# Kernel optimization log

Hardware: AMD Instinct MI355X
Metric: run time of the kernel (lower is better)

Reference implementation:

```python
import jax, jax.numpy as jnp
import numpy as np

D_STATE = 16
D_CONV = 4


def rmsnorm(x, w, eps=1e-6):
    # normalize over last (channel) axis
    return x * jax.lax.rsqrt(jnp.mean(x * x, axis=-1, keepdims=True) + eps) * w


def silu(x):
    return x * jax.nn.sigmoid(x)


def mamba(x, in_proj_w, conv1d_w, conv1d_b, x_proj_w, dt_proj_w, dt_proj_b, A_log, D_param, out_proj_w):
    # x: [B, L, C], d_inner == C (expand=1)
    B, L, C = x.shape
    dt_rank = dt_proj_w.shape[1]
    xz = jnp.einsum('blc,ec->ble', x, in_proj_w)  # [B, L, 2C]
    u, z = jnp.split(xz, 2, axis=-1)
    # causal depthwise conv1d over time (pad left d_conv-1)
    uc = jax.lax.conv_general_dilated(
        u.transpose(0, 2, 1), conv1d_w[:, None, :], (1,), [(D_CONV - 1, 0)],
        dimension_numbers=('NCH', 'OIH', 'NCH'), feature_group_count=C)
    u = silu((uc + conv1d_b[None, :, None]).transpose(0, 2, 1))  # [B, L, C]
    x_dbl = jnp.einsum('blc,ec->ble', u, x_proj_w)  # [B, L, dt_rank + 2*N]
    dt, Bm, Cm = jnp.split(x_dbl, [dt_rank, dt_rank + D_STATE], axis=-1)
    delta = jax.nn.softplus(jnp.einsum('blr,dr->bld', dt, dt_proj_w) + dt_proj_b)  # [B, L, C]
    A = -jnp.exp(A_log)  # [C, N]
    deltaA = jnp.exp(delta[..., None] * A)              # [B, L, C, N]
    deltaBu = (delta * u)[..., None] * Bm[:, :, None, :]  # [B, L, C, N]

    def step(h, inp):
        dA, dBu, c = inp
        h = dA * h + dBu
        return h, jnp.einsum('bdn,bn->bd', h, c)

    h0 = jnp.zeros((B, C, D_STATE), x.dtype)
    _, ys = jax.lax.scan(step, h0, (deltaA.transpose(1, 0, 2, 3),
                                    deltaBu.transpose(1, 0, 2, 3),
                                    Cm.transpose(1, 0, 2)))
    y = ys.transpose(1, 0, 2) + u * D_param  # [B, L, C]
    y = y * silu(z)
    return jnp.einsum('bld,od->blo', y, out_proj_w)


def reference(x, norm_w, in_proj_w, conv1d_w, conv1d_b, x_proj_w, dt_proj_w, dt_proj_b,
              A_log, D_param, out_proj_w, scale_mod, dw_w, dw_b, res_scale):
    B, C, H, W = x.shape
    x_cl = x.transpose(0, 2, 3, 1)              # [B, H, W, C]
    xn_cl = rmsnorm(x_cl, norm_w)
    x_norm = xn_cl.transpose(0, 3, 1, 2)        # [B, C, H, W]
    # bidirectional Mamba over flattened spatial sequence
    x_flat = xn_cl.reshape(B, H * W, C)
    mparams = (in_proj_w, conv1d_w, conv1d_b, x_proj_w, dt_proj_w, dt_proj_b, A_log, D_param, out_proj_w)
    fwd = mamba(x_flat, *mparams)
    bwd = jnp.flip(mamba(jnp.flip(x_flat, axis=1), *mparams), axis=1)
    g = (fwd + bwd) * scale_mod
    global_feat = g.reshape(B, H, W, C).transpose(0, 3, 1, 2)
    # local spatial gating: sigmoid(depthwise 3x3 conv) * x_norm
    conv = jax.lax.conv_general_dilated(
        x_norm, dw_w[:, None, :, :], (1, 1), [(1, 1), (1, 1)],
        dimension_numbers=('NCHW', 'OIHW', 'NCHW'), feature_group_count=C)
    local_feat = jax.nn.sigmoid(conv + dw_b[None, :, None, None]) * x_norm
    return x + res_scale * (global_feat + local_feat)


def setup_inputs() -> dict:
    key = jax.random.key(0)
    ks = jax.random.split(key, 10)
    B, C, H, W = 8, 384, 32, 32
    dt_rank = 24  # ceil(384 / 16)
    s = 0.02
    f32 = jnp.float32
    return {
        'x': jax.random.normal(ks[0], (B, C, H, W), f32),
        'norm_w': jnp.ones((C,), f32),
        'in_proj_w': jax.random.normal(ks[1], (2 * C, C), f32) * s,
        'conv1d_w': jax.random.normal(ks[2], (C, D_CONV), f32) * 0.2,
        'conv1d_b': jnp.zeros((C,), f32),
        'x_proj_w': jax.random.normal(ks[3], (dt_rank + 2 * D_STATE, C), f32) * s,
        'dt_proj_w': jax.random.normal(ks[4], (C, dt_rank), f32) * 0.1,
        'dt_proj_b': jax.random.uniform(ks[5], (C,), f32, -4.0, -2.0),
        'A_log': jnp.log(jnp.tile(jnp.arange(1, D_STATE + 1, dtype=f32), (C, 1))),
        'D_param': jnp.ones((C,), f32),
        'out_proj_w': jax.random.normal(ks[6], (C, C), f32) * s,
        'scale_mod': jnp.full((1,), 0.25, f32),
        'dw_w': jax.random.normal(ks[7], (C, 3, 3), f32) * 0.1,
        'dw_b': jnp.zeros((C,), f32),
        'res_scale': jnp.full((1,), 0.5, f32),
    }
```

## Files before the change

kernel.cpp:

```cpp
#include <hip/hip_runtime.h>
#include <hip/hip_bf16.h>


typedef __attribute__((ext_vector_type(8))) short bf16x8;
typedef __attribute__((ext_vector_type(8))) unsigned short u16x8;
typedef __attribute__((ext_vector_type(4))) float f32x4;

#define L2E 1.44269504088896340736f

static __device__ __forceinline__ unsigned short f2bf(float f) {
  unsigned int u = __builtin_bit_cast(unsigned int, f);
  u += 0x7fff + ((u >> 16) & 1);
  return (unsigned short)(u >> 16);
}
static __device__ __forceinline__ float bf2f(unsigned short u) {
  unsigned int v = (unsigned int)u << 16;
  return __builtin_bit_cast(float, v);
}

__global__ __launch_bounds__(256) void prep_k(
    const float* __restrict__ in_w, const float* __restrict__ x_w,
    const float* __restrict__ dt_w, const float* __restrict__ out_w,
    const float* __restrict__ A_log, const float* __restrict__ nw,
    unsigned short* __restrict__ W_in, unsigned short* __restrict__ W_x,
    unsigned short* __restrict__ W_dt, unsigned short* __restrict__ W_out,
    float* __restrict__ A2) {
  int idx = blockIdx.x * 256 + threadIdx.x;
  switch (blockIdx.y) {
    case 0: if (idx < 768 * 384) W_in[idx] = f2bf(in_w[idx] * nw[idx % 384]); break;
    case 1: if (idx < 64 * 384) { int n = idx / 384, k = idx - n * 384;
              W_x[idx] = f2bf(n < 56 ? x_w[n * 384 + k] : 0.f); } break;
    case 2: if (idx < 384 * 32) { int n = idx >> 5, k = idx & 31;
              W_dt[idx] = f2bf(k < 24 ? dt_w[n * 24 + k] : 0.f); } break;
    case 3: if (idx < 384 * 384) W_out[idx] = f2bf(out_w[idx]); break;
    case 4: if (idx < 384 * 16) A2[idx] = -expf(A_log[idx]) * L2E; break;
  }
}

__global__ __launch_bounds__(256) void transpose_k(
    const float* __restrict__ x, unsigned short* __restrict__ xb,
    float* __restrict__ nf) {
  const int b = blockIdx.y;
  const int l0 = blockIdx.x * 32;
  const int tid = threadIdx.x;
  const int cr = tid >> 5, lw = tid & 31;
  const int cj = tid & 63, lr = tid >> 6;
  __shared__ float t64[64][33];
  __shared__ float part[8][33];
  float acc = 0.f;
  for (int cc = 0; cc < 6; ++cc) {
    #pragma unroll
    for (int k = 0; k < 8; ++k) {
      int cp = k * 8 + cr;
      int c = cc * 64 + cp;
      float v = x[(((size_t)(b * 384 + c)) << 10) + l0 + lw];
      t64[cp][lw] = v;
      acc = fmaf(v, v, acc);
    }
    __syncthreads();
    #pragma unroll
    for (int k2 = 0; k2 < 8; ++k2) {
      int ll = lr + 4 * k2;
      xb[((size_t)((b << 10) + l0 + ll)) * 384 + cc * 64 + cj] = f2bf(t64[cj][ll]);
    }
    __syncthreads();
  }
  part[cr][lw] = acc;
  __syncthreads();
  if (tid < 32) {
    float s = part[0][tid] + part[1][tid] + part[2][tid] + part[3][tid] +
              part[4][tid] + part[5][tid] + part[6][tid] + part[7][tid];
    nf[(b << 10) + l0 + tid] = rsqrtf(s * (1.f / 384.f) + 1e-6f);
  }
}

template <int EPI, int SUMIN>
__global__ __launch_bounds__(256) void gemm_k(
    const unsigned short* __restrict__ A0u, const unsigned short* __restrict__ A1u,
    const unsigned short* __restrict__ Bw, int K, int N,
    float* __restrict__ of0, float* __restrict__ of1,
    unsigned short* __restrict__ ob0, unsigned short* __restrict__ ob1,
    const float* __restrict__ aux) {
  const unsigned short* A = blockIdx.z ? A1u : A0u;
  float* outf = blockIdx.z ? of1 : of0;
  unsigned short* outb = blockIdx.z ? ob1 : ob0;
  __shared__ unsigned short As[64][40];
  __shared__ unsigned short Bs[64][40];
  const int n0 = blockIdx.x * 64, m0 = blockIdx.y * 64;
  const int tid = threadIdx.x;
  const int lane = tid & 63, wave = tid >> 6;
  const int wm = wave >> 1, wn = wave & 1;
  const int lrow = tid >> 2, lseg = (tid & 3) * 8;
  const int fr = lane & 15, ks = (lane >> 4) * 8;
  f32x4 acc[2][2] = {};
  for (int k0 = 0; k0 < K; k0 += 32) {
    __syncthreads();
    if (SUMIN) {
      u16x8 va = *(const u16x8*)&A0u[(size_t)(m0 + lrow) * K + k0 + lseg];
      u16x8 vb = *(const u16x8*)&A1u[(size_t)(m0 + lrow) * K + k0 + lseg];
      u16x8 s;
      #pragma unroll
      for (int j = 0; j < 8; ++j) s[j] = f2bf(bf2f(va[j]) + bf2f(vb[j]));
      *(u16x8*)&As[lrow][lseg] = s;
    } else {
      *(bf16x8*)&As[lrow][lseg] = *(const bf16x8*)&A[(size_t)(m0 + lrow) * K + k0 + lseg];
    }
    *(bf16x8*)&Bs[lrow][lseg] = *(const bf16x8*)&Bw[(size_t)(n0 + lrow) * K + k0 + lseg];
    __syncthreads();
    bf16x8 a0 = *(const bf16x8*)&As[wm * 32 + fr][ks];
    bf16x8 a1 = *(const bf16x8*)&As[wm * 32 + 16 + fr][ks];
    bf16x8 b0 = *(const bf16x8*)&Bs[wn * 32 + fr][ks];
    bf16x8 b1 = *(const bf16x8*)&Bs[wn * 32 + 16 + fr][ks];
    acc[0][0] = __builtin_amdgcn_mfma_f32_16x16x32_bf16(a0, b0, acc[0][0], 0, 0, 0);
    acc[0][1] = __builtin_amdgcn_mfma_f32_16x16x32_bf16(a0, b1, acc[0][1], 0, 0, 0);
    acc[1][0] = __builtin_amdgcn_mfma_f32_16x16x32_bf16(a1, b0, acc[1][0], 0, 0, 0);
    acc[1][1] = __builtin_amdgcn_mfma_f32_16x16x32_bf16(a1, b1, acc[1][1], 0, 0, 0);
  }
  #pragma unroll
  for (int mi = 0; mi < 2; ++mi)
    #pragma unroll
    for (int ni = 0; ni < 2; ++ni)
      #pragma unroll
      for (int j = 0; j < 4; ++j) {
        int m = m0 + wm * 32 + mi * 16 + (lane >> 4) * 4 + j;
        int n = n0 + wn * 32 + ni * 16 + (lane & 15);
        float v = acc[mi][ni][j];
        if (EPI == 0) {
          ob0[(size_t)m * N + n] = f2bf(v * aux[m]);
        } else if (EPI == 1) {
          if (n < 24) outb[m * 32 + n] = f2bf(v);
          else if (n < 32) outb[m * 32 + n] = 0;
          if (n >= 24 && n < 56) outf[m * 32 + (n - 24)] = v;
        } else if (EPI == 2) {
          float t = v + aux[n];
          float sp = (t > 20.f) ? t : log1pf(expf(t));
          outb[(size_t)m * N + n] = f2bf(sp);
        } else {
          of0[(size_t)m * N + n] = v * aux[0];
        }
      }
}

__global__ __launch_bounds__(384) void conv_silu_k(
    const unsigned short* __restrict__ xz, const float* __restrict__ cw,
    const float* __restrict__ cb,
    unsigned short* __restrict__ ub0, unsigned short* __restrict__ ub1) {
  const int st = blockIdx.x, b = blockIdx.y, dir = blockIdx.z;
  const int c = threadIdx.x;
  const int s0 = st * 8;
  const float w0 = cw[c * 4 + 0], w1 = cw[c * 4 + 1];
  const float w2 = cw[c * 4 + 2], w3 = cw[c * 4 + 3];
  const float bb = cb[c];
  unsigned short* ub = dir ? ub1 : ub0;
  float xv[11];
  #pragma unroll
  for (int k = 0; k < 11; ++k) {
    int j = s0 - 3 + k;
    float v = 0.f;
    if (j >= 0) {
      int t = dir ? (1023 - j) : j;
      v = bf2f(xz[(size_t)((b << 10) + t) * 768 + c]);
    }
    xv[k] = v;
  }
  #pragma unroll
  for (int s = 0; s < 8; ++s) {
    float a = bb + xv[s] * w0 + xv[s + 1] * w1 + xv[s + 2] * w2 + xv[s + 3] * w3;
    float uv = a * __builtin_amdgcn_rcpf(1.f + __builtin_amdgcn_exp2f(-a * L2E));
    ub[(size_t)((b << 10) + s0 + s) * 384 + c] = f2bf(uv);
  }
}

__global__ __launch_bounds__(512) void scan1_k(
    const unsigned short* __restrict__ de0, const unsigned short* __restrict__ de1,
    const unsigned short* __restrict__ ub0, const unsigned short* __restrict__ ub1,
    const float* __restrict__ bc0, const float* __restrict__ bc1,
    const float* __restrict__ A2,
    float* __restrict__ Pseg, float* __restrict__ Hseg) {
  const int ct = blockIdx.x, b = blockIdx.y;
  const int dir = blockIdx.z >> 4, seg = blockIdx.z & 15;
  const unsigned short* del = dir ? de1 : de0;
  const unsigned short* uu  = dir ? ub1 : ub0;
  const float* bc  = dir ? bc1 : bc0;
  const int tid = threadIdx.x;
  const int lane = tid & 63, wave = tid >> 6;
  const int n = lane & 15, cg = lane >> 4;
  const int cl = wave * 4 + cg;
  const int c = ct * 32 + cl;
  const float a2 = A2[c * 16 + n];
  const size_t base = ((size_t)b << 10) + seg * 64;
  __shared__ __attribute__((aligned(16))) float sd[2][32][20];
  __shared__ __attribute__((aligned(16))) float sdu[2][32][20];
  __shared__ __attribute__((aligned(16))) float sB[2][32][20];
  const int li = tid >> 5, lj = tid & 31;
  unsigned short rd, ru; float rb;
  auto issue = [&](int s0) {
    size_t rowi = base + s0 + li;
    rd = del[rowi * 384 + ct * 32 + lj];
    ru = uu [rowi * 384 + ct * 32 + lj];
    rb = bc [rowi * 32 + lj];
  };
  auto commit = [&](int buf) {
    float dd = bf2f(rd), uv = bf2f(ru);
    sd[buf][lj][li] = dd; sdu[buf][lj][li] = dd * uv; sB[buf][lj][li] = rb;
  };
  issue(0); commit(0);
  float h = 0.f, P = 1.f;
  for (int ch = 0; ch < 4; ++ch) {
    const int cur = ch & 1;
    if (ch + 1 < 4) issue((ch + 1) * 16);
    __syncthreads();
    f32x4 dv[4], duv[4], bmv[4];
    #pragma unroll
    for (int r = 0; r < 4; ++r) {
      dv[r]  = *(const f32x4*)&sd[cur][cl][r * 4];
      duv[r] = *(const f32x4*)&sdu[cur][cl][r * 4];
      bmv[r] = *(const f32x4*)&sB[cur][n][r * 4];
    }
    #pragma unroll
    for (int i = 0; i < 16; ++i) {
      float dA = __builtin_amdgcn_exp2f(dv[i >> 2][i & 3] * a2);
      h = fmaf(dA, h, duv[i >> 2][i & 3] * bmv[i >> 2][i & 3]);
      P *= dA;
    }
    if (ch + 1 < 4) { __syncthreads(); commit(cur ^ 1); }
  }
  size_t o = (size_t)((dir * 8 + b) * 16 + seg) * 6144 + c * 16 + n;
  Pseg[o] = P; Hseg[o] = h;
}

__global__ __launch_bounds__(256) void scomb_k(
    const float* __restrict__ Pseg, const float* __restrict__ Hseg,
    float* __restrict__ Hin) {
  const int db = blockIdx.y;
  const int r = blockIdx.x * 256 + threadIdx.x;
  float h = 0.f;
  #pragma unroll
  for (int s = 0; s < 16; ++s) {
    size_t o = (size_t)(db * 16 + s) * 6144 + r;
    Hin[o] = h;
    h = Pseg[o] * h + Hseg[o];
  }
}

__global__ __launch_bounds__(512) void scan2_k(
    const unsigned short* __restrict__ de0, const unsigned short* __restrict__ de1,
    const unsigned short* __restrict__ ub0, const unsigned short* __restrict__ ub1,
    const float* __restrict__ bc0, const float* __restrict__ bc1,
    const unsigned short* __restrict__ xz, const float* __restrict__ A2,
    const float* __restrict__ Dp, const float* __restrict__ Hin,
    unsigned short* __restrict__ Sb0, unsigned short* __restrict__ Sb1) {
  const int ct = blockIdx.x, b = blockIdx.y;
  const int dir = blockIdx.z >> 4, seg = blockIdx.z & 15;
  const unsigned short* del = dir ? de1 : de0;
  const unsigned short* uu  = dir ? ub1 : ub0;
  const float* bc  = dir ? bc1 : bc0;
  unsigned short* S = dir ? Sb1 : Sb0;
  const int tid = threadIdx.x;
  const int lane = tid & 63, wave = tid >> 6;
  const int n = lane & 15, cg = lane >> 4;
  const int cl = wave * 4 + cg;
  const int c = ct * 32 + cl;
  const float a2 = A2[c * 16 + n];
  const float dpc = Dp[c];
  const size_t base = (size_t)b << 10;
  const int segoff = seg * 64;
  __shared__ __attribute__((aligned(16))) float sd[2][32][20];
  __shared__ __attribute__((aligned(16))) float sdu[2][32][20];
  __shared__ __attribute__((aligned(16))) float su[2][32][20];
  __shared__ __attribute__((aligned(16))) float sz[2][32][20];
  __shared__ __attribute__((aligned(16))) float sbc[2][32][20];
  const int li = tid >> 5, lj = tid & 31;
  unsigned short rd, ru, rz; float rb;
  auto issue = [&](int s0) {
    size_t rowi = base + segoff + s0 + li;
    rd = del[rowi * 384 + ct * 32 + lj];
    ru = uu [rowi * 384 + ct * 32 + lj];
    int t = dir ? (1023 - (segoff + s0 + li)) : (segoff + s0 + li);
    rz = xz[(base + t) * 768 + 384 + ct * 32 + lj];
    rb = bc[rowi * 32 + lj];
  };
  auto commit = [&](int buf) {
    float dd = bf2f(rd), uv = bf2f(ru);
    sd[buf][lj][li] = dd; sdu[buf][lj][li] = dd * uv;
    su[buf][lj][li] = uv; sz[buf][lj][li] = bf2f(rz);
    sbc[buf][lj][li] = rb;
  };
  issue(0); commit(0);
  float h = Hin[(size_t)((dir * 8 + b) * 16 + seg) * 6144 + c * 16 + n];
  for (int ch = 0; ch < 4; ++ch) {
    const int cur = ch & 1;
    if (ch + 1 < 4) issue((ch + 1) * 16);
    __syncthreads();
    f32x4 dv[4], duv[4], bmv[4], cmv[4];
    #pragma unroll
    for (int r = 0; r < 4; ++r) {
      dv[r]  = *(const f32x4*)&sd[cur][cl][r * 4];
      duv[r] = *(const f32x4*)&sdu[cur][cl][r * 4];
      bmv[r] = *(const f32x4*)&sbc[cur][n][r * 4];
      cmv[r] = *(const f32x4*)&sbc[cur][16 + n][r * 4];
    }
    float p[16];
    #pragma unroll
    for (int i = 0; i < 16; ++i) {
      float dA = __builtin_amdgcn_exp2f(dv[i >> 2][i & 3] * a2);
      h = fmaf(dA, h, duv[i >> 2][i & 3] * bmv[i >> 2][i & 3]);
      p[i] = h * cmv[i >> 2][i & 3];
    }
    float q8[8];
    #pragma unroll
    for (int j = 0; j < 8; ++j) {
      float send = (n & 8) ? p[j] : p[j + 8];
      float recv = __shfl_xor(send, 8);
      float keep = (n & 8) ? p[j + 8] : p[j];
      q8[j] = keep + recv;
    }
    float q4[4];
    #pragma unroll
    for (int j = 0; j < 4; ++j) {
      float send = (n & 4) ? q8[j] : q8[j + 4];
      float recv = __shfl_xor(send, 4);
      float keep = (n & 4) ? q8[j + 4] : q8[j];
      q4[j] = keep + recv;
    }
    float q2[2];
    #pragma unroll
    for (int j = 0; j < 2; ++j) {
      float send = (n & 2) ? q4[j] : q4[j + 2];
      float recv = __shfl_xor(send, 2);
      float keep = (n & 2) ? q4[j + 2] : q4[j];
      q2[j] = keep + recv;
    }
    float send = (n & 1) ? q2[0] : q2[1];
    float recv = __shfl_xor(send, 1);
    float keep = (n & 1) ? q2[1] : q2[0];
    float ysum = keep + recv;
    float uvn = su[cur][cl][n];
    float zz  = sz[cur][cl][n];
    float sig = __builtin_amdgcn_rcpf(1.f + __builtin_amdgcn_exp2f(-zz * L2E));
    float y = (ysum + uvn * dpc) * (zz * sig);
    int s = segoff + ch * 16 + n;
    int t = dir ? (1023 - s) : s;
    S[(base + t) * 384 + c] = f2bf(y);
    if (ch + 1 < 4) { __syncthreads(); commit(cur ^ 1); }
  }
}

__global__ __launch_bounds__(256) void final_k(
    const float* __restrict__ G, const unsigned short* __restrict__ xb,
    const float* __restrict__ nf, const float* __restrict__ nw,
    const float* __restrict__ x, const float* __restrict__ dww,
    const float* __restrict__ dwb, const float* __restrict__ rs,
    float* __restrict__ out) {
  __shared__ float tile[64][33];
  __shared__ float wq[9][64];
  __shared__ float bbs[64], nws[64];
  const int l0 = blockIdx.x * 32, c0 = blockIdx.y * 64, b = blockIdx.z;
  const int tid = threadIdx.x;
  for (int i = tid; i < 576; i += 256) {
    int c = i / 9, q = i - c * 9;
    wq[q][c] = dww[(size_t)(c0 + c) * 9 + q] * nw[c0 + c];
  }
  if (tid < 64) { bbs[tid] = dwb[c0 + tid]; nws[tid] = nw[c0 + tid]; }
  __syncthreads();
  {
    const int oct = tid & 7, li = tid >> 3;
    const int l = l0 + li;
    const int hh = l >> 5, ww = l & 31;
    float acc[8];
    {
      f32x4 ba = *(const f32x4*)&bbs[oct * 8];
      f32x4 bb2 = *(const f32x4*)&bbs[oct * 8 + 4];
      #pragma unroll
      for (int j = 0; j < 4; ++j) { acc[j] = ba[j]; acc[j + 4] = bb2[j]; }
    }
    #pragma unroll
    for (int di = -1; di <= 1; ++di) {
      int h2 = hh + di;
      if (h2 < 0 || h2 > 31) continue;
      #pragma unroll
      for (int dj = -1; dj <= 1; ++dj) {
        int w2 = ww + dj;
        if (w2 < 0 || w2 > 31) continue;
        int lp = h2 * 32 + w2;
        float nfl = nf[(b << 10) + lp];
        u16x8 v = *(const u16x8*)&xb[(size_t)((b << 10) + lp) * 384 + c0 + oct * 8];
        int q = (di + 1) * 3 + (dj + 1);
        f32x4 wa = *(const f32x4*)&wq[q][oct * 8];
        f32x4 wb = *(const f32x4*)&wq[q][oct * 8 + 4];
        #pragma unroll
        for (int j = 0; j < 4; ++j) {
          acc[j]     = fmaf(bf2f(v[j]) * nfl, wa[j], acc[j]);
          acc[j + 4] = fmaf(bf2f(v[j + 4]) * nfl, wb[j], acc[j + 4]);
        }
      }
    }
    size_t ri = (size_t)((b << 10) + l) * 384 + c0 + oct * 8;
    float nfl0 = nf[(b << 10) + l];
    u16x8 xc = *(const u16x8*)&xb[ri];
    f32x4 g0 = *(const f32x4*)&G[ri];
    f32x4 g1 = *(const f32x4*)&G[ri + 4];
    #pragma unroll
    for (int j = 0; j < 8; ++j) {
      float xv = bf2f(xc[j]) * nfl0 * nws[oct * 8 + j];
      float sig = __builtin_amdgcn_rcpf(1.f + __builtin_amdgcn_exp2f(-acc[j] * L2E));
      float gg = (j < 4) ? g0[j] : g1[j - 4];
      tile[oct * 8 + j][li] = gg + xv * sig;
    }
  }
  __syncthreads();
  {
    const int lw = tid & 31, cr = tid >> 5;
    const float rsv = rs[0];
    for (int p = 0; p < 8; ++p) {
      int c = c0 + p * 8 + cr;
      size_t o = ((size_t)(b * 384 + c) << 10) + l0 + lw;
      out[o] = x[o] + rsv * tile[p * 8 + cr][lw];
    }
  }
}

extern "C" void kernel_launch(void* const* d_in, const int* in_sizes, int n_in,
                              void* d_out, int out_size, void* d_ws, size_t ws_size,
                              hipStream_t stream) {
  const float* x         = (const float*)d_in[0];
  const float* norm_w    = (const float*)d_in[1];
  const float* in_proj_w = (const float*)d_in[2];
  const float* conv1d_w  = (const float*)d_in[3];
  const float* conv1d_b  = (const float*)d_in[4];
  const float* x_proj_w  = (const float*)d_in[5];
  const float* dt_proj_w = (const float*)d_in[6];
  const float* dt_proj_b = (const float*)d_in[7];
  const float* A_log     = (const float*)d_in[8];
  const float* D_param   = (const float*)d_in[9];
  const float* out_proj_w= (const float*)d_in[10];
  const float* scale_mod = (const float*)d_in[11];
  const float* dw_w      = (const float*)d_in[12];
  const float* dw_b      = (const float*)d_in[13];
  const float* res_scale = (const float*)d_in[14];
  float* out = (float*)d_out;

  char* base = (char*)d_ws;
  size_t off = 0;
  auto alloc = [&](size_t bytes) {
    off = (off + 255) & ~(size_t)255;
    void* p = base + off;
    off += bytes;
    return p;
  };
  const size_t B_BLC = (size_t)8192 * 384 * 2;

  unsigned short* xb   = (unsigned short*)alloc(B_BLC);
  float*          nf   = (float*)alloc((size_t)8192 * 4);
  unsigned short* xz   = (unsigned short*)alloc((size_t)8192 * 768 * 2);
  unsigned short* u_b0 = (unsigned short*)alloc(B_BLC);
  unsigned short* u_b1 = (unsigned short*)alloc(B_BLC);
  unsigned short* dtp0 = (unsigned short*)alloc((size_t)8192 * 32 * 2);
  unsigned short* dtp1 = (unsigned short*)alloc((size_t)8192 * 32 * 2);
  float*          bc0  = (float*)alloc((size_t)8192 * 32 * 4);
  float*          bc1  = (float*)alloc((size_t)8192 * 32 * 4);
  unsigned short* de0  = (unsigned short*)alloc(B_BLC);
  unsigned short* de1  = (unsigned short*)alloc(B_BLC);
  unsigned short* Sb0  = (unsigned short*)alloc(B_BLC);
  unsigned short* Sb1  = (unsigned short*)alloc(B_BLC);
  float*          Pseg = (float*)alloc((size_t)1572864 * 4);
  float*          Hseg = (float*)alloc((size_t)1572864 * 4);
  float*          Hin  = (float*)alloc((size_t)1572864 * 4);
  unsigned short* W_in = (unsigned short*)alloc((size_t)768 * 384 * 2);
  unsigned short* W_x  = (unsigned short*)alloc((size_t)64 * 384 * 2);
  unsigned short* W_dt = (unsigned short*)alloc((size_t)384 * 32 * 2);
  unsigned short* W_out= (unsigned short*)alloc((size_t)384 * 384 * 2);
  float*          A2   = (float*)alloc((size_t)384 * 16 * 4);
  float*          G    = (float*)alloc((size_t)8192 * 384 * 4);

  prep_k<<<dim3(1152, 5), 256, 0, stream>>>(in_proj_w, x_proj_w, dt_proj_w,
                                            out_proj_w, A_log, norm_w,
                                            W_in, W_x, W_dt, W_out, A2);
  transpose_k<<<dim3(32, 8), 256, 0, stream>>>(x, xb, nf);
  gemm_k<0, 0><<<dim3(12, 128), 256, 0, stream>>>(xb, xb, W_in, 384, 768,
                                                  nullptr, nullptr, xz, xz, nf);
  conv_silu_k<<<dim3(128, 8, 2), 384, 0, stream>>>(xz, conv1d_w, conv1d_b,
                                                   u_b0, u_b1);
  gemm_k<1, 0><<<dim3(1, 128, 2), 256, 0, stream>>>(u_b0, u_b1, W_x, 384, 64,
                                                    bc0, bc1, dtp0, dtp1, nullptr);
  gemm_k<2, 0><<<dim3(6, 128, 2), 256, 0, stream>>>(dtp0, dtp1, W_dt, 32, 384,
                                                    nullptr, nullptr, de0, de1,
                                                    dt_proj_b);
  scan1_k<<<dim3(12, 8, 32), 512, 0, stream>>>(de0, de1, u_b0, u_b1, bc0, bc1,
                                               A2, Pseg, Hseg);
  scomb_k<<<dim3(24, 16), 256, 0, stream>>>(Pseg, Hseg, Hin);
  scan2_k<<<dim3(12, 8, 32), 512, 0, stream>>>(de0, de1, u_b0, u_b1, bc0, bc1,
                                               xz, A2, D_param, Hin, Sb0, Sb1);
  gemm_k<3, 1><<<dim3(6, 128), 256, 0, stream>>>(Sb0, Sb1, W_out, 384, 384,
                                                 G, G, nullptr, nullptr,
                                                 scale_mod);
  final_k<<<dim3(32, 6, 8), 256, 0, stream>>>(G, xb, nf, norm_w, x, dw_w, dw_b,
                                              res_scale, out);
}
```

Baseline: 257.8 us.

## Use 128x128 MFMA GEMM with direct LDS loads, fold scan combine into scan2

Adds a 128x128-tile bf16 MFMA GEMM that moves A/B tiles straight into LDS with global_load_lds and computes a 4x4 fragment grid per wave. It is used for the in_proj and out_proj GEMMs to raise data reuse and arithmetic intensity. The scan kernels now load a whole 64-step segment into LDS once instead of double-buffering 16-step chunks, and compute delta*u on the fly. The separate segment-combine kernel is removed: scan2 rebuilds its starting state from packed (P,h) pairs of the earlier segments, which cuts a launch at the cost of redundant per-thread work and fewer CTAs for the GEMMs.

Result: faster. 247.3 us (-4.0%).

```diff
diff --git a/kernel.cpp b/kernel.cpp
--- a/kernel.cpp
+++ b/kernel.cpp
@@ -17,6 +17,11 @@
   unsigned int v = (unsigned int)u << 16;
   return __builtin_bit_cast(float, v);
 }
+
+#define GLOAD_LDS16(g, l)                                             \
+  __builtin_amdgcn_global_load_lds(                                   \
+      (const __attribute__((address_space(1))) unsigned int*)(g),     \
+      (__attribute__((address_space(3))) unsigned int*)(l), 16, 0, 0)
 
 __global__ __launch_bounds__(256) void prep_k(
     const float* __restrict__ in_w, const float* __restrict__ x_w,
@@ -75,6 +80,81 @@
 }
 
 template <int EPI, int SUMIN>
+__global__ __launch_bounds__(256) void gemm128_k(
+    const unsigned short* __restrict__ A0u, const unsigned short* __restrict__ A1u,
+    const unsigned short* __restrict__ Bw, int K, int N,
+    float* __restrict__ outf, unsigned short* __restrict__ outb,
+    const float* __restrict__ aux) {
+  __shared__ __attribute__((aligned(16))) unsigned short As[128 * 32];
+  __shared__ __attribute__((aligned(16))) unsigned short Bs[128 * 32];
+  const int n0 = blockIdx.x * 128, m0 = blockIdx.y * 128;
+  const int tid = threadIdx.x;
+  const int lane = tid & 63, wave = tid >> 6;
+  const int wm = wave >> 1, wn = wave & 1;
+  const int fr = lane & 15, ks = (lane >> 4) * 8;
+  const int row = tid >> 2, colseg = (tid & 3) * 8;
+  const unsigned short* pA0 = A0u + (size_t)(m0 + row) * K + colseg;
+  const unsigned short* pA1 = A0u + (size_t)(m0 + 64 + row) * K + colseg;
+  const unsigned short* pB0 = Bw + (size_t)(n0 + row) * K + colseg;
+  const unsigned short* pB1 = Bw + (size_t)(n0 + 64 + row) * K + colseg;
+  unsigned short* lA0 = As + wave * 512;
+  unsigned short* lA1 = As + 2048 + wave * 512;
+  unsigned short* lB0 = Bs + wave * 512;
+  unsigned short* lB1 = Bs + 2048 + wave * 512;
+  f32x4 acc[4][4] = {};
+  for (int k0 = 0; k0 < K; k0 += 32) {
+    __syncthreads();
+    if (SUMIN) {
+      #pragma unroll
+      for (int p = 0; p < 2; ++p) {
+        int r = p * 64 + row;
+        u16x8 va = *(const u16x8*)&A0u[(size_t)(m0 + r) * K + k0 + colseg];
+        u16x8 vb = *(const u16x8*)&A1u[(size_t)(m0 + r) * K + k0 + colseg];
+        u16x8 s;
+        #pragma unroll
+        for (int j = 0; j < 8; ++j) s[j] = f2bf(bf2f(va[j]) + bf2f(vb[j]));
+        *(u16x8*)&As[r * 32 + colseg] = s;
+      }
+    } else {
+      GLOAD_LDS16(pA0, lA0);
+      GLOAD_LDS16(pA1, lA1);
+      pA0 += 32; pA1 += 32;
+    }
+    GLOAD_LDS16(pB0, lB0);
+    GLOAD_LDS16(pB1, lB1);
+    pB0 += 32; pB1 += 32;
+    __syncthreads();
+    bf16x8 af[4], bf[4];
+    #pragma unroll
+    for (int mi = 0; mi < 4; ++mi)
+      af[mi] = *(const bf16x8*)&As[(wm * 64 + mi * 16 + fr) * 32 + ks];
+    #pragma unroll
+    for (int ni = 0; ni < 4; ++ni)
+      bf[ni] = *(const bf16x8*)&Bs[(wn * 64 + ni * 16 + fr) * 32 + ks];
+    #pragma unroll
+    for (int mi = 0; mi < 4; ++mi)
+      #pragma unroll
+      for (int ni = 0; ni < 4; ++ni)
+        acc[mi][ni] = __builtin_amdgcn_mfma_f32_16x16x32_bf16(af[mi], bf[ni], acc[mi][ni], 0, 0, 0);
+  }
+  #pragma unroll
+  for (int mi = 0; mi < 4; ++mi)
+    #pragma unroll
+    for (int ni = 0; ni < 4; ++ni)
+      #pragma unroll
+      for (int j = 0; j < 4; ++j) {
+        int m = m0 + wm * 64 + mi * 16 + (lane >> 4) * 4 + j;
+        int n = n0 + wn * 64 + ni * 16 + fr;
+        float v = acc[mi][ni][j];
+        if (EPI == 0) {
+          outb[(size_t)m * N + n] = f2bf(v * aux[m]);
+        } else {
+          outf[(size_t)m * N + n] = v * aux[0];
+        }
+      }
+}
+
+template <int EPI>
 __global__ __launch_bounds__(256) void gemm_k(
     const unsigned short* __restrict__ A0u, const unsigned short* __restrict__ A1u,
     const unsigned short* __restrict__ Bw, int K, int N,
@@ -95,16 +175,7 @@
   f32x4 acc[2][2] = {};
   for (int k0 = 0; k0 < K; k0 += 32) {
     __syncthreads();
-    if (SUMIN) {
-      u16x8 va = *(const u16x8*)&A0u[(size_t)(m0 + lrow) * K + k0 + lseg];
-      u16x8 vb = *(const u16x8*)&A1u[(size_t)(m0 + lrow) * K + k0 + lseg];
-      u16x8 s;
-      #pragma unroll
-      for (int j = 0; j < 8; ++j) s[j] = f2bf(bf2f(va[j]) + bf2f(vb[j]));
-      *(u16x8*)&As[lrow][lseg] = s;
-    } else {
-      *(bf16x8*)&As[lrow][lseg] = *(const bf16x8*)&A[(size_t)(m0 + lrow) * K + k0 + lseg];
-    }
+    *(bf16x8*)&As[lrow][lseg] = *(const bf16x8*)&A[(size_t)(m0 + lrow) * K + k0 + lseg];
     *(bf16x8*)&Bs[lrow][lseg] = *(const bf16x8*)&Bw[(size_t)(n0 + lrow) * K + k0 + lseg];
     __syncthreads();
     bf16x8 a0 = *(const bf16x8*)&As[wm * 32 + fr][ks];
@@ -125,18 +196,14 @@
         int m = m0 + wm * 32 + mi * 16 + (lane >> 4) * 4 + j;
         int n = n0 + wn * 32 + ni * 16 + (lane & 15);
         float v = acc[mi][ni][j];
-        if (EPI == 0) {
-          ob0[(size_t)m * N + n] = f2bf(v * aux[m]);
-        } else if (EPI == 1) {
+        if (EPI == 1) {
           if (n < 24) outb[m * 32 + n] = f2bf(v);
           else if (n < 32) outb[m * 32 + n] = 0;
           if (n >= 24 && n < 56) outf[m * 32 + (n - 24)] = v;
-        } else if (EPI == 2) {
+        } else {
           float t = v + aux[n];
           float sp = (t > 20.f) ? t : log1pf(expf(t));
           outb[(size_t)m * N + n] = f2bf(sp);
-        } else {
-          of0[(size_t)m * N + n] = v * aux[0];
         }
       }
 }
@@ -175,8 +242,7 @@
     const unsigned short* __restrict__ de0, const unsigned short* __restrict__ de1,
     const unsigned short* __restrict__ ub0, const unsigned short* __restrict__ ub1,
     const float* __restrict__ bc0, const float* __restrict__ bc1,
-    const float* __restrict__ A2,
-    float* __restrict__ Pseg, float* __restrict__ Hseg) {
+    const float* __restrict__ A2, float* __restrict__ PH) {
   const int ct = blockIdx.x, b = blockIdx.y;
   const int dir = blockIdx.z >> 4, seg = blockIdx.z & 15;
   const unsigned short* del = dir ? de1 : de0;
@@ -189,58 +255,49 @@
   const int c = ct * 32 + cl;
   const float a2 = A2[c * 16 + n];
   const size_t base = ((size_t)b << 10) + seg * 64;
-  __shared__ __attribute__((aligned(16))) float sd[2][32][20];
-  __shared__ __attribute__((aligned(16))) float sdu[2][32][20];
-  __shared__ __attribute__((aligned(16))) float sB[2][32][20];
+  __shared__ __attribute__((aligned(16))) float sd[32][68];
+  __shared__ __attribute__((aligned(16))) float su[32][68];
+  __shared__ __attribute__((aligned(16))) float sB[16][68];
   const int li = tid >> 5, lj = tid & 31;
-  unsigned short rd, ru; float rb;
-  auto issue = [&](int s0) {
-    size_t rowi = base + s0 + li;
-    rd = del[rowi * 384 + ct * 32 + lj];
-    ru = uu [rowi * 384 + ct * 32 + lj];
-    rb = bc [rowi * 32 + lj];
-  };
-  auto commit = [&](int buf) {
-    float dd = bf2f(rd), uv = bf2f(ru);
-    sd[buf][lj][li] = dd; sdu[buf][lj][li] = dd * uv; sB[buf][lj][li] = rb;
-  };
-  issue(0); commit(0);
+  const int li3 = tid >> 4, lj3 = tid & 15;
+  unsigned short rd[4], ru[4];
+  float rb[2];
+  #pragma unroll
+  for (int k = 0; k < 4; ++k) {
+    size_t rowi = base + k * 16 + li;
+    rd[k] = del[rowi * 384 + ct * 32 + lj];
+    ru[k] = uu [rowi * 384 + ct * 32 + lj];
+  }
+  #pragma unroll
+  for (int k = 0; k < 2; ++k)
+    rb[k] = bc[(base + k * 32 + li3) * 32 + lj3];
+  #pragma unroll
+  for (int k = 0; k < 4; ++k) {
+    sd[lj][k * 16 + li] = bf2f(rd[k]);
+    su[lj][k * 16 + li] = bf2f(ru[k]);
+  }
+  #pragma unroll
+  for (int k = 0; k < 2; ++k) sB[lj3][k * 32 + li3] = rb[k];
+  __syncthreads();
   float h = 0.f, P = 1.f;
   for (int ch = 0; ch < 4; ++ch) {
-    const int cur = ch & 1;
-    if (ch + 1 < 4) issue((ch + 1) * 16);
-    __syncthreads();
-    f32x4 dv[4], duv[4], bmv[4];
+    f32x4 dv[4], uv4[4], bmv[4];
     #pragma unroll
     for (int r = 0; r < 4; ++r) {
-      dv[r]  = *(const f32x4*)&sd[cur][cl][r * 4];
-      duv[r] = *(const f32x4*)&sdu[cur][cl][r * 4];
-      bmv[r] = *(const f32x4*)&sB[cur][n][r * 4];
+      dv[r]  = *(const f32x4*)&sd[cl][ch * 16 + r * 4];
+      uv4[r] = *(const f32x4*)&su[cl][ch * 16 + r * 4];
+      bmv[r] = *(const f32x4*)&sB[n][ch * 16 + r * 4];
     }
     #pragma unroll
     for (int i = 0; i < 16; ++i) {
-      float dA = __builtin_amdgcn_exp2f(dv[i >> 2][i & 3] * a2);
-      h = fmaf(dA, h, duv[i >> 2][i & 3] * bmv[i >> 2][i & 3]);
+      float dd = dv[i >> 2][i & 3];
+      float dA = __builtin_amdgcn_exp2f(dd * a2);
+      h = fmaf(dA, h, dd * uv4[i >> 2][i & 3] * bmv[i >> 2][i & 3]);
       P *= dA;
     }
-    if (ch + 1 < 4) { __syncthreads(); commit(cur ^ 1); }
   }
   size_t o = (size_t)((dir * 8 + b) * 16 + seg) * 6144 + c * 16 + n;
-  Pseg[o] = P; Hseg[o] = h;
-}
-
-__global__ __launch_bounds__(256) void scomb_k(
-    const float* __restrict__ Pseg, const float* __restrict__ Hseg,
-    float* __restrict__ Hin) {
-  const int db = blockIdx.y;
-  const int r = blockIdx.x * 256 + threadIdx.x;
-  float h = 0.f;
-  #pragma unroll
-  for (int s = 0; s < 16; ++s) {
-    size_t o = (size_t)(db * 16 + s) * 6144 + r;
-    Hin[o] = h;
-    h = Pseg[o] * h + Hseg[o];
-  }
+  *(float2*)&PH[o * 2] = make_float2(P, h);
 }
 
 __global__ __launch_bounds__(512) void scan2_k(
@@ -248,7 +305,7 @@
     const unsigned short* __restrict__ ub0, const unsigned short* __restrict__ ub1,
     const float* __restrict__ bc0, const float* __restrict__ bc1,
     const unsigned short* __restrict__ xz, const float* __restrict__ A2,
-    const float* __restrict__ Dp, const float* __restrict__ Hin,
+    const float* __restrict__ Dp, const float* __restrict__ PH,
     unsigned short* __restrict__ Sb0, unsigned short* __restrict__ Sb1) {
   const int ct = blockIdx.x, b = blockIdx.y;
   const int dir = blockIdx.z >> 4, seg = blockIdx.z & 15;
@@ -265,46 +322,54 @@
   const float dpc = Dp[c];
   const size_t base = (size_t)b << 10;
   const int segoff = seg * 64;
-  __shared__ __attribute__((aligned(16))) float sd[2][32][20];
-  __shared__ __attribute__((aligned(16))) float sdu[2][32][20];
-  __shared__ __attribute__((aligned(16))) float su[2][32][20];
-  __shared__ __attribute__((aligned(16))) float sz[2][32][20];
-  __shared__ __attribute__((aligned(16))) float sbc[2][32][20];
+  __shared__ __attribute__((aligned(16))) float sd[32][68];
+  __shared__ __attribute__((aligned(16))) float su[32][68];
+  __shared__ __attribute__((aligned(16))) float sz[32][68];
+  __shared__ __attribute__((aligned(16))) float sbc[32][68];
   const int li = tid >> 5, lj = tid & 31;
-  unsigned short rd, ru, rz; float rb;
-  auto issue = [&](int s0) {
-    size_t rowi = base + segoff + s0 + li;
-    rd = del[rowi * 384 + ct * 32 + lj];
-    ru = uu [rowi * 384 + ct * 32 + lj];
-    int t = dir ? (1023 - (segoff + s0 + li)) : (segoff + s0 + li);
-    rz = xz[(base + t) * 768 + 384 + ct * 32 + lj];
-    rb = bc[rowi * 32 + lj];
-  };
-  auto commit = [&](int buf) {
-    float dd = bf2f(rd), uv = bf2f(ru);
-    sd[buf][lj][li] = dd; sdu[buf][lj][li] = dd * uv;
-    su[buf][lj][li] = uv; sz[buf][lj][li] = bf2f(rz);
-    sbc[buf][lj][li] = rb;
-  };
-  issue(0); commit(0);
-  float h = Hin[(size_t)((dir * 8 + b) * 16 + seg) * 6144 + c * 16 + n];
+  unsigned short rd[4], ru[4], rz[4];
+  float rb[4];
+  #pragma unroll
+  for (int k = 0; k < 4; ++k) {
+    size_t rowi = base + segoff + k * 16 + li;
+    rd[k] = del[rowi * 384 + ct * 32 + lj];
+    ru[k] = uu [rowi * 384 + ct * 32 + lj];
+    int t = dir ? (1023 - (segoff + k * 16 + li)) : (segoff + k * 16 + li);
+    rz[k] = xz[(base + t) * 768 + 384 + ct * 32 + lj];
+    rb[k] = bc[rowi * 32 + lj];
+  }
+  float h = 0.f;
+  {
+    size_t rb2 = ((size_t)((dir * 8 + b) * 16) * 6144 + c * 16 + n) * 2;
+    #pragma unroll
+    for (int s = 0; s < 15; ++s) {
+      float2 ph = *(const float2*)&PH[rb2 + (size_t)s * 12288];
+      h = (s < seg) ? fmaf(ph.x, h, ph.y) : h;
+    }
+  }
+  #pragma unroll
+  for (int k = 0; k < 4; ++k) {
+    sd[lj][k * 16 + li] = bf2f(rd[k]);
+    su[lj][k * 16 + li] = bf2f(ru[k]);
+    sz[lj][k * 16 + li] = bf2f(rz[k]);
+    sbc[lj][k * 16 + li] = rb[k];
+  }
+  __syncthreads();
   for (int ch = 0; ch < 4; ++ch) {
-    const int cur = ch & 1;
-    if (ch + 1 < 4) issue((ch + 1) * 16);
-    __syncthreads();
-    f32x4 dv[4], duv[4], bmv[4], cmv[4];
+    f32x4 dv[4], uv4[4], bmv[4], cmv[4];
     #pragma unroll
     for (int r = 0; r < 4; ++r) {
-      dv[r]  = *(const f32x4*)&sd[cur][cl][r * 4];
-      duv[r] = *(const f32x4*)&sdu[cur][cl][r * 4];
-      bmv[r] = *(const f32x4*)&sbc[cur][n][r * 4];
-      cmv[r] = *(const f32x4*)&sbc[cur][16 + n][r * 4];
+      dv[r]  = *(const f32x4*)&sd[cl][ch * 16 + r * 4];
+      uv4[r] = *(const f32x4*)&su[cl][ch * 16 + r * 4];
+      bmv[r] = *(const f32x4*)&sbc[n][ch * 16 + r * 4];
+      cmv[r] = *(const f32x4*)&sbc[16 + n][ch * 16 + r * 4];
     }
     float p[16];
     #pragma unroll
     for (int i = 0; i < 16; ++i) {
-      float dA = __builtin_amdgcn_exp2f(dv[i >> 2][i & 3] * a2);
-      h = fmaf(dA, h, duv[i >> 2][i & 3] * bmv[i >> 2][i & 3]);
+      float dd = dv[i >> 2][i & 3];
+      float dA = __builtin_amdgcn_exp2f(dd * a2);
+      h = fmaf(dA, h, dd * uv4[i >> 2][i & 3] * bmv[i >> 2][i & 3]);
       p[i] = h * cmv[i >> 2][i & 3];
     }
     float q8[8];
@@ -335,14 +400,13 @@
     float recv = __shfl_xor(send, 1);
     float keep = (n & 1) ? q2[1] : q2[0];
     float ysum = keep + recv;
-    float uvn = su[cur][cl][n];
-    float zz  = sz[cur][cl][n];
+    float uvn = su[cl][ch * 16 + n];
+    float zz  = sz[cl][ch * 16 + n];
     float sig = __builtin_amdgcn_rcpf(1.f + __builtin_amdgcn_exp2f(-zz * L2E));
     float y = (ysum + uvn * dpc) * (zz * sig);
     int s = segoff + ch * 16 + n;
     int t = dir ? (1023 - s) : s;
     S[(base + t) * 384 + c] = f2bf(y);
-    if (ch + 1 < 4) { __syncthreads(); commit(cur ^ 1); }
   }
 }
 
@@ -463,9 +527,7 @@
   unsigned short* de1  = (unsigned short*)alloc(B_BLC);
   unsigned short* Sb0  = (unsigned short*)alloc(B_BLC);
   unsigned short* Sb1  = (unsigned short*)alloc(B_BLC);
-  float*          Pseg = (float*)alloc((size_t)1572864 * 4);
-  float*          Hseg = (float*)alloc((size_t)1572864 * 4);
-  float*          Hin  = (float*)alloc((size_t)1572864 * 4);
+  float*          PH   = (float*)alloc((size_t)1572864 * 2 * 4);
   unsigned short* W_in = (unsigned short*)alloc((size_t)768 * 384 * 2);
   unsigned short* W_x  = (unsigned short*)alloc((size_t)64 * 384 * 2);
   unsigned short* W_dt = (unsigned short*)alloc((size_t)384 * 32 * 2);
@@ -477,23 +539,21 @@
                                             out_proj_w, A_log, norm_w,
                                             W_in, W_x, W_dt, W_out, A2);
   transpose_k<<<dim3(32, 8), 256, 0, stream>>>(x, xb, nf);
-  gemm_k<0, 0><<<dim3(12, 128), 256, 0, stream>>>(xb, xb, W_in, 384, 768,
-                                                  nullptr, nullptr, xz, xz, nf);
+  gemm128_k<0, 0><<<dim3(6, 64), 256, 0, stream>>>(xb, xb, W_in, 384, 768,
+                                                   nullptr, xz, nf);
   conv_silu_k<<<dim3(128, 8, 2), 384, 0, stream>>>(xz, conv1d_w, conv1d_b,
                                                    u_b0, u_b1);
-  gemm_k<1, 0><<<dim3(1, 128, 2), 256, 0, stream>>>(u_b0, u_b1, W_x, 384, 64,
-                                                    bc0, bc1, dtp0, dtp1, nullptr);
-  gemm_k<2, 0><<<dim3(6, 128, 2), 256, 0, stream>>>(dtp0, dtp1, W_dt, 32, 384,
-                                                    nullptr, nullptr, de0, de1,
-                                                    dt_proj_b);
+  gemm_k<1><<<dim3(1, 128, 2), 256, 0, stream>>>(u_b0, u_b1, W_x, 384, 64,
+                                                 bc0, bc1, dtp0, dtp1, nullptr);
+  gemm_k<2><<<dim3(6, 128, 2), 256, 0, stream>>>(dtp0, dtp1, W_dt, 32, 384,
+                                                 nullptr, nullptr, de0, de1,
+                                                 dt_proj_b);
   scan1_k<<<dim3(12, 8, 32), 512, 0, stream>>>(de0, de1, u_b0, u_b1, bc0, bc1,
-                                               A2, Pseg, Hseg);
-  scomb_k<<<dim3(24, 16), 256, 0, stream>>>(Pseg, Hseg, Hin);
+                                               A2, PH);
   scan2_k<<<dim3(12, 8, 32), 512, 0, stream>>>(de0, de1, u_b0, u_b1, bc0, bc1,
-                                               xz, A2, D_param, Hin, Sb0, Sb1);
-  gemm_k<3, 1><<<dim3(6, 128), 256, 0, stream>>>(Sb0, Sb1, W_out, 384, 384,
-                                                 G, G, nullptr, nullptr,
-                                                 scale_mod);
+                                               xz, A2, D_param, PH, Sb0, Sb1);
+  gemm128_k<3, 1><<<dim3(3, 64), 256, 0, stream>>>(Sb0, Sb1, W_out, 384, 384,
+                                                   G, nullptr, scale_mod);
   final_k<<<dim3(32, 6, 8), 256, 0, stream>>>(G, xb, nf, norm_w, x, dw_w, dw_b,
                                               res_scale, out);
 }
```
